# Kernel tuning notes

Measured on AMD Instinct MI355X. Metric: run time of the kernel, lower is better.

## Reference

```python
import jax, jax.numpy as jnp
import numpy as np

N_NODES = 1_000_000
N_EDGES = 16_000_000
N_IN, HID, N_OUT = 128, 32, 16


def setup_inputs() -> dict:
    key = jax.random.key(0)
    ks = jax.random.split(key, 8)
    x = jax.random.normal(ks[0], (N_NODES, N_IN), dtype=jnp.float32)
    edge_index = jax.random.randint(ks[1], (2, N_EDGES), 0, N_NODES, dtype=jnp.int64)
    edge_weight = jax.random.uniform(ks[2], (N_EDGES,), dtype=jnp.float32)
    # ChebConv(K=1) parameters: one linear per layer + bias
    def glorot(k, fan_in, fan_out):
        s = jnp.sqrt(6.0 / (fan_in + fan_out))
        return jax.random.uniform(k, (fan_in, fan_out), minval=-s, maxval=s, dtype=jnp.float32)
    W0 = glorot(ks[3], N_IN, HID)
    b0 = jnp.zeros((HID,), dtype=jnp.float32)
    W1 = glorot(ks[4], HID, HID)
    b1 = jnp.zeros((HID,), dtype=jnp.float32)
    W2 = glorot(ks[5], HID, N_OUT)
    b2 = jnp.zeros((N_OUT,), dtype=jnp.float32)
    return {"x": x, "edge_index": edge_index, "edge_weight": edge_weight,
            "W0": W0, "b0": b0, "W1": W1, "b1": b1, "W2": W2, "b2": b2}


def reference(x, edge_index, edge_weight, W0, b0, W1, b1, W2, b2):
    # PyG ChebConv with K=1: out = lins[0](Tx_0) + bias, Tx_0 = x.
    # The Laplacian propagation over edge_index/edge_weight is only used for K>=2,
    # so edge_index/edge_weight do not enter the math (kept for signature fidelity).
    h = jax.nn.relu(x @ W0 + b0)      # ChebConv1 + relu
    h = jax.nn.relu(h @ W1 + b1)      # ChebConv2 + relu
    # Dropout(p=0.0) is identity
    return h @ W2 + b2                # ChebConv3 -> [N, nOutputs]
```

## Files before the change

kernel.cpp:

```cpp
#include <hip/hip_runtime.h>
#include <stdint.h>


#define N_IN  128
#define HID   32
#define N_OUT 16

using f32x4  = __attribute__((ext_vector_type(4))) float;
using short8 = __attribute__((ext_vector_type(8))) short;
using uint4v = __attribute__((ext_vector_type(4))) unsigned int;

#define N_CHUNKS 22
#define TOTAL_WF_SHORTS (N_CHUNKS * 512)
#define WLDS_GRANULES (N_CHUNKS * 64)

__device__ __forceinline__ unsigned fu(float f) {
    union { float f; unsigned u; } v; v.f = f; return v.u;
}
__device__ __forceinline__ float uf(unsigned u) {
    union { unsigned u; float f; } v; v.u = u; return v.f;
}
__device__ __forceinline__ unsigned short f2bf_rne(float f) {
    unsigned u = fu(f);
    return (unsigned short)((u + 0x7fffu + ((u >> 16) & 1u)) >> 16);
}

__global__ void split_weights(const float* __restrict__ W0,
                              const float* __restrict__ W1,
                              const float* __restrict__ W2,
                              unsigned short* __restrict__ wf) {
    int idx = blockIdx.x * blockDim.x + threadIdx.x;
    if (idx >= TOTAL_WF_SHORTS) return;
    int chunk  = idx >> 9;
    int within = idx & 511;
    int lane = within >> 3;
    int j    = within & 7;
    const float* W; int ncol, k, col, hl;
    if (chunk < 16) {
        int kc = chunk >> 2, nh = (chunk >> 1) & 1; hl = chunk & 1;
        k = kc * 32 + 8 * (lane >> 4) + j; col = nh * 16 + (lane & 15);
        W = W0; ncol = HID;
    } else if (chunk < 20) {
        int c2 = chunk - 16, nh = c2 >> 1; hl = c2 & 1;
        k = 8 * (lane >> 4) + j; col = nh * 16 + (lane & 15);
        W = W1; ncol = HID;
    } else {
        hl = chunk - 20;
        k = 8 * (lane >> 4) + j; col = lane & 15;
        W = W2; ncol = N_OUT;
    }
    float v = W[k * ncol + col];
    unsigned hi_bits = fu(v) & 0xFFFF0000u;
    wf[idx] = (hl == 0) ? (unsigned short)(hi_bits >> 16)
                        : f2bf_rne(v - uf(hi_bits));
}

#define MFMA3(acc, ah, al, bh, bl)                                          \
    do {                                                                    \
        acc = __builtin_amdgcn_mfma_f32_16x16x32_bf16(ah, bh, acc, 0, 0, 0);\
        acc = __builtin_amdgcn_mfma_f32_16x16x32_bf16(al, bh, acc, 0, 0, 0);\
        acc = __builtin_amdgcn_mfma_f32_16x16x32_bf16(ah, bl, acc, 0, 0, 0);\
    } while (0)

#define GAS1(p) ((const unsigned int __attribute__((address_space(1)))*)(uintptr_t)(p))
#define LAS3(p) ((unsigned int __attribute__((address_space(3)))*)(uintptr_t)(p))

__global__ __launch_bounds__(256, 1) void gnn_mfma(
    const float* __restrict__ x, const unsigned short* __restrict__ wf,
    const float* __restrict__ b0, const float* __restrict__ b1,
    const float* __restrict__ b2, float* __restrict__ out,
    int n_tiles, int stride)
{
    __shared__ __align__(16) unsigned short wlds[N_CHUNKS * 512];
    __shared__ __align__(16) unsigned short hbuf[4][2][16][40];
    __shared__ __align__(16) float xbuf[4][2][2048];

    const int tid  = threadIdx.x;
    const int wave = tid >> 6;
    const int l    = tid & 63;
    const int r16  = l & 15;
    const int g    = l >> 4;

    {
        const uint4v* wfv = reinterpret_cast<const uint4v*>(wf);
        uint4v* wl = reinterpret_cast<uint4v*>(wlds);
        for (int gg = tid; gg < WLDS_GRANULES; gg += 256)
            wl[gg] = wfv[gg];
    }
    __syncthreads();

    const short8* WL = reinterpret_cast<const short8*>(wlds);

    const float bc0a = b0[r16], bc0b = b0[16 + r16];
    const float bc1a = b1[r16], bc1b = b1[16 + r16];
    const float bc2  = b2[r16];

    const int gw = blockIdx.x * 4 + wave;

    const int srow = l >> 5;
    const int st   = l & 31;

    #define STAGE(buf, tileidx)                                                \
    do {                                                                       \
        const float* sb_ = x + (size_t)(tileidx) * 16 * N_IN;                  \
        _Pragma("unroll")                                                      \
        for (int i_ = 0; i_ < 8; ++i_) {                                       \
            int row_ = i_ * 2 + srow;                                          \
            const float* src_ = sb_ + row_ * N_IN + ((st ^ row_) << 2);        \
            float* dst_ = &xbuf[wave][buf][i_ * 256];                          \
            __builtin_amdgcn_global_load_lds(GAS1(src_), LAS3(dst_), 16, 0, 0);\
        }                                                                      \
    } while (0)

    int b = 0;
    STAGE(0, gw);

    for (int tile = gw; tile < n_tiles; tile += stride) {
        const int nb = tile * 16;

        asm volatile("s_waitcnt vmcnt(0)" ::: "memory");
        __builtin_amdgcn_sched_barrier(0);

        f32x4 xa[4], xbv[4];
        {
            const f32x4* rb = reinterpret_cast<const f32x4*>(&xbuf[wave][b][r16 * 128]);
            #pragma unroll
            for (int kc = 0; kc < 4; ++kc) {
                int t0 = g * 2 + kc * 8;
                xa[kc]  = rb[t0 ^ r16];
                xbv[kc] = rb[(t0 + 1) ^ r16];
            }
        }

        {
            int ntt = tile + stride;
            int pf = (ntt < n_tiles) ? ntt : tile;
            STAGE(b ^ 1, pf);
        }

        f32x4 acc0 = {0.f, 0.f, 0.f, 0.f};
        f32x4 acc1 = {0.f, 0.f, 0.f, 0.f};

        #pragma unroll
        for (int kc = 0; kc < 4; ++kc) {
            float f[8] = {xa[kc][0], xa[kc][1], xa[kc][2], xa[kc][3],
                          xbv[kc][0], xbv[kc][1], xbv[kc][2], xbv[kc][3]};
            uint4v hv, lv;
            #pragma unroll
            for (int p = 0; p < 4; ++p) {
                unsigned u0 = fu(f[2 * p]), u1 = fu(f[2 * p + 1]);
                unsigned h0b = u0 & 0xFFFF0000u, h1b = u1 & 0xFFFF0000u;
                hv[p] = h1b | (u0 >> 16);
                float l0 = f[2 * p] - uf(h0b), l1 = f[2 * p + 1] - uf(h1b);
                lv[p] = (fu(l1) & 0xFFFF0000u) | (fu(l0) >> 16);
            }
            short8 ah = __builtin_bit_cast(short8, hv);
            short8 al = __builtin_bit_cast(short8, lv);
            short8 w0h0 = WL[(kc * 4 + 0) * 64 + l];
            short8 w0l0 = WL[(kc * 4 + 1) * 64 + l];
            short8 w0h1 = WL[(kc * 4 + 2) * 64 + l];
            short8 w0l1 = WL[(kc * 4 + 3) * 64 + l];
            MFMA3(acc0, ah, al, w0h0, w0l0);
            MFMA3(acc1, ah, al, w0h1, w0l1);
        }

        #pragma unroll
        for (int i = 0; i < 4; ++i) {
            int row = 4 * g + i;
            float h = fmaxf(acc0[i] + bc0a, 0.f);
            unsigned hb = fu(h) & 0xFFFF0000u;
            hbuf[wave][0][row][r16] = (unsigned short)(hb >> 16);
            hbuf[wave][1][row][r16] = (unsigned short)(fu(h - uf(hb)) >> 16);
            float h2 = fmaxf(acc1[i] + bc0b, 0.f);
            unsigned hb2 = fu(h2) & 0xFFFF0000u;
            hbuf[wave][0][row][16 + r16] = (unsigned short)(hb2 >> 16);
            hbuf[wave][1][row][16 + r16] = (unsigned short)(fu(h2 - uf(hb2)) >> 16);
        }
        short8 h0h = *reinterpret_cast<const short8*>(&hbuf[wave][0][r16][g * 8]);
        short8 h0l = *reinterpret_cast<const short8*>(&hbuf[wave][1][r16][g * 8]);

        f32x4 acc2 = {0.f, 0.f, 0.f, 0.f};
        f32x4 acc3 = {0.f, 0.f, 0.f, 0.f};
        {
            short8 w1h0 = WL[(16 + 0) * 64 + l];
            short8 w1l0 = WL[(16 + 1) * 64 + l];
            short8 w1h1 = WL[(16 + 2) * 64 + l];
            short8 w1l1 = WL[(16 + 3) * 64 + l];
            MFMA3(acc2, h0h, h0l, w1h0, w1l0);
            MFMA3(acc3, h0h, h0l, w1h1, w1l1);
        }
        #pragma unroll
        for (int i = 0; i < 4; ++i) {
            int row = 4 * g + i;
            float h = fmaxf(acc2[i] + bc1a, 0.f);
            unsigned hb = fu(h) & 0xFFFF0000u;
            hbuf[wave][0][row][r16] = (unsigned short)(hb >> 16);
            hbuf[wave][1][row][r16] = (unsigned short)(fu(h - uf(hb)) >> 16);
            float h2 = fmaxf(acc3[i] + bc1b, 0.f);
            unsigned hb2 = fu(h2) & 0xFFFF0000u;
            hbuf[wave][0][row][16 + r16] = (unsigned short)(hb2 >> 16);
            hbuf[wave][1][row][16 + r16] = (unsigned short)(fu(h2 - uf(hb2)) >> 16);
        }
        short8 h1h = *reinterpret_cast<const short8*>(&hbuf[wave][0][r16][g * 8]);
        short8 h1l = *reinterpret_cast<const short8*>(&hbuf[wave][1][r16][g * 8]);

        f32x4 accO = {0.f, 0.f, 0.f, 0.f};
        {
            short8 w2h = WL[(20) * 64 + l];
            short8 w2l = WL[(21) * 64 + l];
            MFMA3(accO, h1h, h1l, w2h, w2l);
        }
        #pragma unroll
        for (int i = 0; i < 4; ++i) {
            int row = 4 * g + i;
            __builtin_nontemporal_store(
                accO[i] + bc2, out + (size_t)(nb + row) * N_OUT + r16);
        }

        b ^= 1;
    }
    #undef STAGE
}

extern "C" void kernel_launch(void* const* d_in, const int* in_sizes, int n_in,
                              void* d_out, int out_size, void* d_ws, size_t ws_size,
                              hipStream_t stream) {
    const float* x  = (const float*)d_in[0];
    const float* W0 = (const float*)d_in[3];
    const float* b0 = (const float*)d_in[4];
    const float* W1 = (const float*)d_in[5];
    const float* b1 = (const float*)d_in[6];
    const float* W2 = (const float*)d_in[7];
    const float* b2 = (const float*)d_in[8];
    float* out = (float*)d_out;
    unsigned short* wf = (unsigned short*)d_ws;

    int n_nodes = in_sizes[0] / N_IN;
    int n_tiles = n_nodes / 16;

    split_weights<<<(TOTAL_WF_SHORTS + 255) / 256, 256, 0, stream>>>(W0, W1, W2, wf);

    const int n_blocks = 256;
    const int n_waves_total = n_blocks * 4;
    gnn_mfma<<<dim3(n_blocks), dim3(256), 0, stream>>>(
        x, wf, b0, b1, b2, out, n_tiles, n_waves_total);
}
```

Baseline: 113.6 us.

## Swap MFMA operand roles to keep hidden activations in registers

Weights become the A operand and activations the B operand of each MFMA, so each lane's accumulator holds feature values for a single node. The weight pre-split permutes rows to match this layout. That lets the split of each layer's output feed the next layer straight from registers, with no per-wave LDS staging buffer. The final output is written as one 16-byte store per lane instead of four scalar stores. The cost is a more intricate weight permutation whose correctness depends on matching the MFMA lane mapping exactly.

```diff
diff --git a/kernel.cpp b/kernel.cpp
--- a/kernel.cpp
+++ b/kernel.cpp
@@ -35,31 +35,47 @@
     int within = idx & 511;
     int lane = within >> 3;
     int j    = within & 7;
-    const float* W; int ncol, k, col, hl;
+    int g4   = 4 * (lane >> 4);
+    int r16  = lane & 15;
+    int rho  = (j < 4) ? (g4 + j) : (16 + g4 + (j - 4));
+    float v; int hl;
     if (chunk < 16) {
-        int kc = chunk >> 2, nh = (chunk >> 1) & 1; hl = chunk & 1;
-        k = kc * 32 + 8 * (lane >> 4) + j; col = nh * 16 + (lane & 15);
-        W = W0; ncol = HID;
+        int kc = chunk >> 2, b = (chunk >> 1) & 1; hl = chunk & 1;
+        int k = kc * 32 + 2 * g4 + j;
+        v = W0[k * HID + 16 * b + r16];
     } else if (chunk < 20) {
-        int c2 = chunk - 16, nh = c2 >> 1; hl = c2 & 1;
-        k = 8 * (lane >> 4) + j; col = nh * 16 + (lane & 15);
-        W = W1; ncol = HID;
+        int c2 = chunk - 16, b = c2 >> 1; hl = c2 & 1;
+        v = W1[rho * HID + 16 * b + r16];
     } else {
         hl = chunk - 20;
-        k = 8 * (lane >> 4) + j; col = lane & 15;
-        W = W2; ncol = N_OUT;
+        v = W2[rho * N_OUT + r16];
     }
-    float v = W[k * ncol + col];
     unsigned hi_bits = fu(v) & 0xFFFF0000u;
     wf[idx] = (hl == 0) ? (unsigned short)(hi_bits >> 16)
                         : f2bf_rne(v - uf(hi_bits));
 }
 
-#define MFMA3(acc, ah, al, bh, bl)                                          \
+#define MFMA3(acc, wh, wl, xh, xl)                                          \
     do {                                                                    \
-        acc = __builtin_amdgcn_mfma_f32_16x16x32_bf16(ah, bh, acc, 0, 0, 0);\
-        acc = __builtin_amdgcn_mfma_f32_16x16x32_bf16(al, bh, acc, 0, 0, 0);\
-        acc = __builtin_amdgcn_mfma_f32_16x16x32_bf16(ah, bl, acc, 0, 0, 0);\
+        acc = __builtin_amdgcn_mfma_f32_16x16x32_bf16(wh, xh, acc, 0, 0, 0);\
+        acc = __builtin_amdgcn_mfma_f32_16x16x32_bf16(wl, xh, acc, 0, 0, 0);\
+        acc = __builtin_amdgcn_mfma_f32_16x16x32_bf16(wh, xl, acc, 0, 0, 0);\
+    } while (0)
+
+#define SPLIT8A(farr, AH, AL)                                               \
+    do {                                                                    \
+        uint4v hv_, lv_;                                                    \
+        _Pragma("unroll")                                                   \
+        for (int p_ = 0; p_ < 4; ++p_) {                                    \
+            unsigned u0_ = fu((farr)[2 * p_]), u1_ = fu((farr)[2 * p_ + 1]);\
+            unsigned h0_ = u0_ & 0xFFFF0000u, h1_ = u1_ & 0xFFFF0000u;      \
+            hv_[p_] = h1_ | (u0_ >> 16);                                    \
+            float l0_ = (farr)[2 * p_] - uf(h0_);                           \
+            float l1_ = (farr)[2 * p_ + 1] - uf(h1_);                       \
+            lv_[p_] = (fu(l1_) & 0xFFFF0000u) | (fu(l0_) >> 16);            \
+        }                                                                   \
+        AH = __builtin_bit_cast(short8, hv_);                               \
+        AL = __builtin_bit_cast(short8, lv_);                               \
     } while (0)
 
 #define GAS1(p) ((const unsigned int __attribute__((address_space(1)))*)(uintptr_t)(p))
@@ -72,7 +88,6 @@
     int n_tiles, int stride)
 {
     __shared__ __align__(16) unsigned short wlds[N_CHUNKS * 512];
-    __shared__ __align__(16) unsigned short hbuf[4][2][16][40];
     __shared__ __align__(16) float xbuf[4][2][2048];
 
     const int tid  = threadIdx.x;
@@ -91,9 +106,11 @@
 
     const short8* WL = reinterpret_cast<const short8*>(wlds);
 
-    const float bc0a = b0[r16], bc0b = b0[16 + r16];
-    const float bc1a = b1[r16], bc1b = b1[16 + r16];
-    const float bc2  = b2[r16];
+    const f32x4 bb0a = *reinterpret_cast<const f32x4*>(b0 + 4 * g);
+    const f32x4 bb0b = *reinterpret_cast<const f32x4*>(b0 + 16 + 4 * g);
+    const f32x4 bb1a = *reinterpret_cast<const f32x4*>(b1 + 4 * g);
+    const f32x4 bb1b = *reinterpret_cast<const f32x4*>(b1 + 16 + 4 * g);
+    const f32x4 bb2  = *reinterpret_cast<const f32x4*>(b2 + 4 * g);
 
     const int gw = blockIdx.x * 4 + wave;
 
@@ -145,39 +162,24 @@
         for (int kc = 0; kc < 4; ++kc) {
             float f[8] = {xa[kc][0], xa[kc][1], xa[kc][2], xa[kc][3],
                           xbv[kc][0], xbv[kc][1], xbv[kc][2], xbv[kc][3]};
-            uint4v hv, lv;
-            #pragma unroll
-            for (int p = 0; p < 4; ++p) {
-                unsigned u0 = fu(f[2 * p]), u1 = fu(f[2 * p + 1]);
-                unsigned h0b = u0 & 0xFFFF0000u, h1b = u1 & 0xFFFF0000u;
-                hv[p] = h1b | (u0 >> 16);
-                float l0 = f[2 * p] - uf(h0b), l1 = f[2 * p + 1] - uf(h1b);
-                lv[p] = (fu(l1) & 0xFFFF0000u) | (fu(l0) >> 16);
-            }
-            short8 ah = __builtin_bit_cast(short8, hv);
-            short8 al = __builtin_bit_cast(short8, lv);
+            short8 xh, xl;
+            SPLIT8A(f, xh, xl);
             short8 w0h0 = WL[(kc * 4 + 0) * 64 + l];
             short8 w0l0 = WL[(kc * 4 + 1) * 64 + l];
             short8 w0h1 = WL[(kc * 4 + 2) * 64 + l];
             short8 w0l1 = WL[(kc * 4 + 3) * 64 + l];
-            MFMA3(acc0, ah, al, w0h0, w0l0);
-            MFMA3(acc1, ah, al, w0h1, w0l1);
-        }
-
+            MFMA3(acc0, w0h0, w0l0, xh, xl);
+            MFMA3(acc1, w0h1, w0l1, xh, xl);
+        }
+
+        float hf[8];
         #pragma unroll
         for (int i = 0; i < 4; ++i) {
-            int row = 4 * g + i;
-            float h = fmaxf(acc0[i] + bc0a, 0.f);
-            unsigned hb = fu(h) & 0xFFFF0000u;
-            hbuf[wave][0][row][r16] = (unsigned short)(hb >> 16);
-            hbuf[wave][1][row][r16] = (unsigned short)(fu(h - uf(hb)) >> 16);
-            float h2 = fmaxf(acc1[i] + bc0b, 0.f);
-            unsigned hb2 = fu(h2) & 0xFFFF0000u;
-            hbuf[wave][0][row][16 + r16] = (unsigned short)(hb2 >> 16);
-            hbuf[wave][1][row][16 + r16] = (unsigned short)(fu(h2 - uf(hb2)) >> 16);
-        }
-        short8 h0h = *reinterpret_cast<const short8*>(&hbuf[wave][0][r16][g * 8]);
-        short8 h0l = *reinterpret_cast<const short8*>(&hbuf[wave][1][r16][g * 8]);
+            hf[i]     = fmaxf(acc0[i] + bb0a[i], 0.f);
+            hf[4 + i] = fmaxf(acc1[i] + bb0b[i], 0.f);
+        }
+        short8 hbh, hbl;
+        SPLIT8A(hf, hbh, hbl);
 
         f32x4 acc2 = {0.f, 0.f, 0.f, 0.f};
         f32x4 acc3 = {0.f, 0.f, 0.f, 0.f};
@@ -186,36 +188,30 @@
             short8 w1l0 = WL[(16 + 1) * 64 + l];
             short8 w1h1 = WL[(16 + 2) * 64 + l];
             short8 w1l1 = WL[(16 + 3) * 64 + l];
-            MFMA3(acc2, h0h, h0l, w1h0, w1l0);
-            MFMA3(acc3, h0h, h0l, w1h1, w1l1);
-        }
+            MFMA3(acc2, w1h0, w1l0, hbh, hbl);
+            MFMA3(acc3, w1h1, w1l1, hbh, hbl);
+        }
+        float hf2[8];
         #pragma unroll
         for (int i = 0; i < 4; ++i) {
-            int row = 4 * g + i;
-            float h = fmaxf(acc2[i] + bc1a, 0.f);
-            unsigned hb = fu(h) & 0xFFFF0000u;
-            hbuf[wave][0][row][r16] = (unsigned short)(hb >> 16);
-            hbuf[wave][1][row][r16] = (unsigned short)(fu(h - uf(hb)) >> 16);
-            float h2 = fmaxf(acc3[i] + bc1b, 0.f);
-            unsigned hb2 = fu(h2) & 0xFFFF0000u;
-            hbuf[wave][0][row][16 + r16] = (unsigned short)(hb2 >> 16);
-            hbuf[wave][1][row][16 + r16] = (unsigned short)(fu(h2 - uf(hb2)) >> 16);
-        }
-        short8 h1h = *reinterpret_cast<const short8*>(&hbuf[wave][0][r16][g * 8]);
-        short8 h1l = *reinterpret_cast<const short8*>(&hbuf[wave][1][r16][g * 8]);
+            hf2[i]     = fmaxf(acc2[i] + bb1a[i], 0.f);
+            hf2[4 + i] = fmaxf(acc3[i] + bb1b[i], 0.f);
+        }
+        short8 h2h, h2l;
+        SPLIT8A(hf2, h2h, h2l);
 
         f32x4 accO = {0.f, 0.f, 0.f, 0.f};
         {
             short8 w2h = WL[(20) * 64 + l];
             short8 w2l = WL[(21) * 64 + l];
-            MFMA3(accO, h1h, h1l, w2h, w2l);
-        }
-        #pragma unroll
-        for (int i = 0; i < 4; ++i) {
-            int row = 4 * g + i;
-            __builtin_nontemporal_store(
-                accO[i] + bc2, out + (size_t)(nb + row) * N_OUT + r16);
-        }
+            MFMA3(accO, w2h, w2l, h2h, h2l);
+        }
+
+        f32x4 ov;
+        #pragma unroll
+        for (int i = 0; i < 4; ++i) ov[i] = accO[i] + bb2[i];
+        __builtin_nontemporal_store(
+            ov, reinterpret_cast<f32x4*>(out + (size_t)(nb + r16) * N_OUT + 4 * g));
 
         b ^= 1;
     }
```

Measured after the change: 111.1 us. 2.1% less time.
